# Kernel optimization log

Hardware: AMD Instinct MI355X
Metric: run time of the kernel (lower is better)

The kernel has to match this reference:

```python
import jax, jax.numpy as jnp
import numpy as np
import math

N_GRAPHS = 25
NODES_PER = 2000
N = N_GRAPHS * NODES_PER      # 50000 total nodes
E = 800000                    # total edges
D = 128                       # hidden = out_dim
VOCAB = 30                    # node_len
NLAYERS = 4                   # gcn_num_layers


def setup_inputs() -> dict:
    key = jax.random.key(0)
    ks = jax.random.split(key, 16)
    labels = jax.random.randint(ks[0], (N,), 0, VOCAB)
    src = jax.random.randint(ks[1], (E,), 0, N)
    dst = jax.random.randint(ks[2], (E,), 0, N)
    # true permutations per graph (as the torch code assumes)
    perms = jax.vmap(lambda k: jax.random.permutation(k, NODES_PER))(
        jax.random.split(ks[3], N_GRAPHS))
    s = 0.02
    emb = jax.random.normal(ks[4], (VOCAB, D)) * s
    Ws = jax.random.normal(ks[5], (NLAYERS, D, D)) * s
    bs = jnp.zeros((NLAYERS, D))
    # MLPReadout(D, D) with L=2: D -> D//2 -> D//4 -> D
    w1 = jax.random.normal(ks[6], (D, D // 2)) * s
    b1 = jnp.zeros((D // 2,))
    w2 = jax.random.normal(ks[7], (D // 2, D // 4)) * s
    b2 = jnp.zeros((D // 4,))
    w3 = jax.random.normal(ks[8], (D // 4, D)) * s
    b3 = jnp.zeros((D,))
    return {"labels": labels, "src": src, "dst": dst, "perms": perms,
            "emb": emb, "Ws": Ws, "bs": bs,
            "w1": w1, "b1": b1, "w2": w2, "b2": b2, "w3": w3, "b3": b3}


def _pos_encoding(perms):
    # sinusoidal table [NODES_PER, D]; position starts at 1 per the torch code
    pos = (jnp.arange(NODES_PER, dtype=jnp.float32) + 1.0)[:, None]       # [n,1]
    div = jnp.exp(jnp.arange(0, D, 2, dtype=jnp.float32)
                  * (-math.log(10000.0) / D))                              # [D/2]
    ang = pos * div                                                        # [n,D/2]
    table = jnp.stack([jnp.sin(ang), jnp.cos(ang)], axis=-1).reshape(NODES_PER, D)
    # pes[i][perm_i] = table  (scatter rows per graph)
    pe = jax.vmap(lambda p: jnp.zeros((NODES_PER, D), jnp.float32).at[p].set(table))(perms)
    return pe.reshape(N, D)


def reference(labels, src, dst, perms, emb, Ws, bs, w1, b1, w2, b2, w3, b3):
    h = emb[labels]                                   # embedding lookup [N,D]
    h = h + _pos_encoding(perms)

    ones = jnp.ones((E,), jnp.float32)
    deg_out = jnp.maximum(jax.ops.segment_sum(ones, src, num_segments=N), 1.0)
    deg_in = jnp.maximum(jax.ops.segment_sum(ones, dst, num_segments=N), 1.0)
    isq_src = deg_out ** -0.5                         # DGL GraphConv norm='both'
    isq_dst = deg_in ** -0.5

    for l in range(NLAYERS):
        hn = h * isq_src[:, None]
        m = jax.ops.segment_sum(hn[src], dst, num_segments=N)  # gather-scatter
        m = m * isq_dst[:, None]
        out = jax.nn.relu(m @ Ws[l] + bs[l])
        h = out + h                                   # residual (all dims equal)

    # MLPReadout: D -> D//2 -> D//4 -> D
    x = jax.nn.relu(h @ w1 + b1)
    x = jax.nn.relu(x @ w2 + b2)
    return x @ w3 + b3                                # [N, D]
```

## Files before the change

kernel.cpp:

```cpp
#include <hip/hip_runtime.h>

#define N_NODES 50000
#define N_EDGES 800000
#define D 128
#define NLAYERS 4
#define NODES_PER 2000
#define CAP 64

typedef __attribute__((ext_vector_type(8))) short bf16x8;
typedef __attribute__((ext_vector_type(4))) float f32x4;

__device__ inline unsigned rne16(float f) {
    unsigned u = __float_as_uint(f);
    return (u + 0x7fffu + ((u >> 16) & 1u)) >> 16;
}
__device__ inline unsigned pack_bf2(float a, float b) {
    return rne16(a) | (rne16(b) << 16);
}
__device__ inline float4 bf4_to_f4(uint2 v) {
    float4 r;
    r.x = __uint_as_float(v.x << 16);
    r.y = __uint_as_float(v.x & 0xffff0000u);
    r.z = __uint_as_float(v.y << 16);
    r.w = __uint_as_float(v.y & 0xffff0000u);
    return r;
}

__global__ void build_kernel(const int* __restrict__ src, const int* __restrict__ dst,
                             int* __restrict__ cursor, int* __restrict__ cnt_out_rep,
                             unsigned short* __restrict__ bucket) {
    int e = blockIdx.x * 256 + threadIdx.x;
    if (e < N_EDGES) {
        int s = src[e], d = dst[e];
        atomicAdd(&cnt_out_rep[(blockIdx.x & 3) * N_NODES + s], 1);
        int pos = atomicAdd(&cursor[d], 1);
        if (pos < CAP) bucket[d * CAP + pos] = (unsigned short)s;
    }
}

__global__ void finalize_kernel(const int* __restrict__ cursor,
                                const int* __restrict__ cnt_out_rep,
                                float* __restrict__ isq_src, float* __restrict__ isq_dst) {
    int i = blockIdx.x * 256 + threadIdx.x;
    if (i < N_NODES) {
        int co = cnt_out_rep[i] + cnt_out_rep[N_NODES + i] +
                 cnt_out_rep[2 * N_NODES + i] + cnt_out_rep[3 * N_NODES + i];
        isq_src[i] = rsqrtf((float)max(co, 1));
        isq_dst[i] = rsqrtf((float)max(cursor[i], 1));
    }
}

__global__ void transpose_w_kernel(const float* __restrict__ Ws,
                                   unsigned short* __restrict__ Wt) {
    int l = blockIdx.x;
    const float* W = Ws + (size_t)l * D * D;
    unsigned short* T = Wt + (size_t)l * D * D;
    for (int i = threadIdx.x; i < D * D; i += 256) {
        int k = i >> 7, n = i & 127;
        T[n * D + k] = (unsigned short)rne16(W[i]);
    }
}

__global__ void init_h_kernel(const int* __restrict__ labels, const int* __restrict__ perms,
                              const float* __restrict__ emb, const float* __restrict__ isq_src,
                              float* __restrict__ h, unsigned short* __restrict__ hs16) {
    int b = blockIdx.x;
    int g = b / NODES_PER;
    int i = b - g * NODES_PER;
    int node = g * NODES_PER + perms[b];
    int d = threadIdx.x;
    int k = d >> 1;
    float ang = (float)(i + 1) * expf((float)(2 * k) * (-9.210340371976184f / 128.0f));
    float pe = (d & 1) ? cosf(ang) : sinf(ang);
    float v = emb[labels[node] * D + d] + pe;
    h[node * D + d] = v;
    hs16[node * D + d] = (unsigned short)rne16(v * isq_src[node]);
}

__global__ __launch_bounds__(256) void aggregate_kernel(const unsigned short* __restrict__ hs16,
        const int* __restrict__ cursor, const unsigned short* __restrict__ bucket,
        const float* __restrict__ isq_dst, unsigned short* __restrict__ m16) {
    int node = blockIdx.x * 4 + (threadIdx.x >> 6);
    int lane = threadIdx.x & 63;
    int q = lane >> 4;
    int col = lane & 15;
    int deg = min(cursor[node], CAP);
    int start = node * CAP;
    int end = start + deg;
    const unsigned short* hb = hs16 + col * 8;
    float a[8] = {0.f, 0.f, 0.f, 0.f, 0.f, 0.f, 0.f, 0.f};

    int e = start;
    for (; e + 8 <= end; e += 8) {
        int s0 = bucket[e + q];
        int s1 = bucket[e + 4 + q];
        uint4 v0 = *(const uint4*)&hb[s0 * D];
        uint4 v1 = *(const uint4*)&hb[s1 * D];
        float4 f0 = bf4_to_f4(make_uint2(v0.x, v0.y));
        float4 f1 = bf4_to_f4(make_uint2(v0.z, v0.w));
        float4 f2 = bf4_to_f4(make_uint2(v1.x, v1.y));
        float4 f3 = bf4_to_f4(make_uint2(v1.z, v1.w));
        a[0] += f0.x; a[1] += f0.y; a[2] += f0.z; a[3] += f0.w;
        a[4] += f1.x; a[5] += f1.y; a[6] += f1.z; a[7] += f1.w;
        a[0] += f2.x; a[1] += f2.y; a[2] += f2.z; a[3] += f2.w;
        a[4] += f3.x; a[5] += f3.y; a[6] += f3.z; a[7] += f3.w;
    }
    if (e + 4 <= end) {
        int s0 = bucket[e + q];
        uint4 v0 = *(const uint4*)&hb[s0 * D];
        float4 f0 = bf4_to_f4(make_uint2(v0.x, v0.y));
        float4 f1 = bf4_to_f4(make_uint2(v0.z, v0.w));
        a[0] += f0.x; a[1] += f0.y; a[2] += f0.z; a[3] += f0.w;
        a[4] += f1.x; a[5] += f1.y; a[6] += f1.z; a[7] += f1.w;
        e += 4;
    }
    int r = end - e;
    if (q < r) {
        int s0 = bucket[e + q];
        uint4 v0 = *(const uint4*)&hb[s0 * D];
        float4 f0 = bf4_to_f4(make_uint2(v0.x, v0.y));
        float4 f1 = bf4_to_f4(make_uint2(v0.z, v0.w));
        a[0] += f0.x; a[1] += f0.y; a[2] += f0.z; a[3] += f0.w;
        a[4] += f1.x; a[5] += f1.y; a[6] += f1.z; a[7] += f1.w;
    }
#pragma unroll
    for (int i = 0; i < 8; ++i) {
        a[i] += __shfl_xor(a[i], 16, 64);
        a[i] += __shfl_xor(a[i], 32, 64);
    }
    if (q == 0) {
        float wd = isq_dst[node];
        uint4 o;
        o.x = pack_bf2(a[0] * wd, a[1] * wd);
        o.y = pack_bf2(a[2] * wd, a[3] * wd);
        o.z = pack_bf2(a[4] * wd, a[5] * wd);
        o.w = pack_bf2(a[6] * wd, a[7] * wd);
        *(uint4*)&m16[node * D + col * 8] = o;
    }
}

__global__ __launch_bounds__(256) void layer_mfma_kernel(const unsigned short* __restrict__ m16,
        const unsigned short* __restrict__ Wt, const float* __restrict__ bias,
        float* __restrict__ h, unsigned short* __restrict__ hs16,
        const float* __restrict__ isq) {
    int wave = threadIdx.x >> 6;
    int lane = threadIdx.x & 63;
    int rowbase = blockIdx.x * 64 + wave * 16;
    int col16 = lane & 15;
    int kq8 = (lane >> 4) * 8;

    int arow = min(rowbase + col16, N_NODES - 1);
    bf16x8 afrag[4];
#pragma unroll
    for (int kk = 0; kk < 4; ++kk)
        afrag[kk] = *(const bf16x8*)&m16[(size_t)arow * D + kk * 32 + kq8];

    int orow0 = rowbase + (lane >> 4) * 4;

#pragma unroll 2
    for (int nt = 0; nt < 8; ++nt) {
        int ncol = nt * 16 + col16;
        float bv = bias[ncol];
        f32x4 acc = {bv, bv, bv, bv};
#pragma unroll
        for (int kk = 0; kk < 4; ++kk) {
            bf16x8 bfrag = *(const bf16x8*)&Wt[(size_t)ncol * D + kk * 32 + kq8];
            acc = __builtin_amdgcn_mfma_f32_16x16x32_bf16(afrag[kk], bfrag, acc, 0, 0, 0);
        }
#pragma unroll
        for (int r = 0; r < 4; ++r) {
            int row = orow0 + r;
            if (row < N_NODES) {
                size_t idx = (size_t)row * D + ncol;
                float o = fmaxf(acc[r], 0.f) + h[idx];
                h[idx] = o;
                if (isq) hs16[idx] = (unsigned short)rne16(o * isq[row]);
            }
        }
    }
}

__global__ __launch_bounds__(256, 4) void readout_kernel(const float* __restrict__ h,
        const float* __restrict__ w1, const float* __restrict__ b1,
        const float* __restrict__ w2, const float* __restrict__ b2,
        const float* __restrict__ w3, const float* __restrict__ b3,
        float* __restrict__ out) {
    __shared__ float hT[128][68];
    int t = threadIdx.x;
    int rowbase = blockIdx.x * 64;
    int tx = t & 15, ty = t >> 4;
    int r0 = ty * 4;

    for (int i = t; i < 2048; i += 256) {
        int row = i >> 5;
        int kc = i & 31;
        int grow = rowbase + row;
        float4 v = (grow < N_NODES) ? *(const float4*)&h[grow * D + kc * 4]
                                    : make_float4(0.f, 0.f, 0.f, 0.f);
        int cs = row ^ ((kc & 7) << 2);
        hT[kc * 4 + 0][cs] = v.x;
        hT[kc * 4 + 1][cs] = v.y;
        hT[kc * 4 + 2][cs] = v.z;
        hT[kc * 4 + 3][cs] = v.w;
    }
    __syncthreads();

    float a1[4][4];
    {
        int c1 = tx * 4;
        float4 bv = *(const float4*)&b1[c1];
#pragma unroll
        for (int i = 0; i < 4; ++i) {
            a1[i][0] = bv.x; a1[i][1] = bv.y; a1[i][2] = bv.z; a1[i][3] = bv.w;
        }
#pragma unroll 2
        for (int k = 0; k < 128; ++k) {
            int s4 = ((k >> 2) & 7) << 2;
            float4 ma = *(const float4*)&hT[k][r0 ^ s4];
            float4 wv = *(const float4*)&w1[k * 64 + c1];
            float mv[4] = {ma.x, ma.y, ma.z, ma.w};
#pragma unroll
            for (int i = 0; i < 4; ++i) {
                a1[i][0] += mv[i] * wv.x;
                a1[i][1] += mv[i] * wv.y;
                a1[i][2] += mv[i] * wv.z;
                a1[i][3] += mv[i] * wv.w;
            }
        }
    }
    __syncthreads();
    {
        int c1 = tx * 4;
#pragma unroll
        for (int j = 0; j < 4; ++j) {
            int c = c1 + j;
            int cs = r0 ^ (((c >> 2) & 7) << 2);
            *(float4*)&hT[c][cs] = make_float4(fmaxf(a1[0][j], 0.f), fmaxf(a1[1][j], 0.f),
                                               fmaxf(a1[2][j], 0.f), fmaxf(a1[3][j], 0.f));
        }
    }
    __syncthreads();

    {
        int c2 = tx * 2;
        float a2[4][2];
        float2 bv = *(const float2*)&b2[c2];
#pragma unroll
        for (int i = 0; i < 4; ++i) { a2[i][0] = bv.x; a2[i][1] = bv.y; }
#pragma unroll 2
        for (int k = 0; k < 64; ++k) {
            int s4 = ((k >> 2) & 7) << 2;
            float4 ma = *(const float4*)&hT[k][r0 ^ s4];
            float2 wv = *(const float2*)&w2[k * 32 + c2];
            float mv[4] = {ma.x, ma.y, ma.z, ma.w};
#pragma unroll
            for (int i = 0; i < 4; ++i) {
                a2[i][0] += mv[i] * wv.x;
                a2[i][1] += mv[i] * wv.y;
            }
        }
#pragma unroll
        for (int j = 0; j < 2; ++j) {
            int c = c2 + j;
            int cs = r0 ^ (((c >> 2) & 7) << 2);
            *(float4*)&hT[64 + c][cs] = make_float4(fmaxf(a2[0][j], 0.f), fmaxf(a2[1][j], 0.f),
                                                    fmaxf(a2[2][j], 0.f), fmaxf(a2[3][j], 0.f));
        }
    }
    __syncthreads();

    {
        int c0 = tx * 8;
        float acc[4][8];
        float4 bv0 = *(const float4*)&b3[c0];
        float4 bv1 = *(const float4*)&b3[c0 + 4];
#pragma unroll
        for (int i = 0; i < 4; ++i) {
            acc[i][0] = bv0.x; acc[i][1] = bv0.y; acc[i][2] = bv0.z; acc[i][3] = bv0.w;
            acc[i][4] = bv1.x; acc[i][5] = bv1.y; acc[i][6] = bv1.z; acc[i][7] = bv1.w;
        }
#pragma unroll 4
        for (int k = 0; k < 32; ++k) {
            int s4 = ((k >> 2) & 7) << 2;
            float4 ma = *(const float4*)&hT[64 + k][r0 ^ s4];
            float4 wa = *(const float4*)&w3[k * D + c0];
            float4 wb = *(const float4*)&w3[k * D + c0 + 4];
            float mv[4] = {ma.x, ma.y, ma.z, ma.w};
            float wv[8] = {wa.x, wa.y, wa.z, wa.w, wb.x, wb.y, wb.z, wb.w};
#pragma unroll
            for (int i = 0; i < 4; ++i)
#pragma unroll
                for (int j = 0; j < 8; ++j)
                    acc[i][j] += mv[i] * wv[j];
        }
#pragma unroll
        for (int i = 0; i < 4; ++i) {
            int row = rowbase + r0 + i;
            if (row < N_NODES) {
                *(float4*)&out[row * D + c0] =
                    make_float4(acc[i][0], acc[i][1], acc[i][2], acc[i][3]);
                *(float4*)&out[row * D + c0 + 4] =
                    make_float4(acc[i][4], acc[i][5], acc[i][6], acc[i][7]);
            }
        }
    }
}

extern "C" void kernel_launch(void* const* d_in, const int* in_sizes, int n_in,
                              void* d_out, int out_size, void* d_ws, size_t ws_size,
                              hipStream_t stream) {
    const int*   labels = (const int*)d_in[0];
    const int*   src    = (const int*)d_in[1];
    const int*   dst    = (const int*)d_in[2];
    const int*   perms  = (const int*)d_in[3];
    const float* emb    = (const float*)d_in[4];
    const float* Ws     = (const float*)d_in[5];
    const float* bs     = (const float*)d_in[6];
    const float* w1     = (const float*)d_in[7];
    const float* b1     = (const float*)d_in[8];
    const float* w2     = (const float*)d_in[9];
    const float* b2     = (const float*)d_in[10];
    const float* w3     = (const float*)d_in[11];
    const float* b3     = (const float*)d_in[12];
    float* out = (float*)d_out;

    char* p = (char*)d_ws;
    auto alloc = [&](size_t bytes) -> char* {
        char* r = p;
        p += (bytes + 255) & ~size_t(255);
        return r;
    };
    float*          h       = (float*)alloc((size_t)N_NODES * D * 4);
    unsigned short* hs16    = (unsigned short*)alloc((size_t)N_NODES * D * 2);
    unsigned short* m16     = (unsigned short*)alloc((size_t)N_NODES * D * 2);
    unsigned short* Wt      = (unsigned short*)alloc((size_t)NLAYERS * D * D * 2);
    float*          isq_src = (float*)alloc((size_t)N_NODES * 4);
    float*          isq_dst = (float*)alloc((size_t)N_NODES * 4);
    int*            cursor  = (int*)alloc((size_t)5 * N_NODES * 4);
    int*            cnt_rep = cursor + N_NODES;
    unsigned short* bucket  = (unsigned short*)alloc((size_t)N_NODES * CAP * 2);

    hipMemsetAsync(cursor, 0, (size_t)5 * N_NODES * 4, stream);
    transpose_w_kernel<<<NLAYERS, 256, 0, stream>>>(Ws, Wt);
    build_kernel<<<(N_EDGES + 255) / 256, 256, 0, stream>>>(src, dst, cursor, cnt_rep, bucket);
    finalize_kernel<<<(N_NODES + 255) / 256, 256, 0, stream>>>(cursor, cnt_rep,
                                                               isq_src, isq_dst);
    init_h_kernel<<<N_NODES, 128, 0, stream>>>(labels, perms, emb, isq_src, h, hs16);

    for (int l = 0; l < NLAYERS; ++l) {
        aggregate_kernel<<<N_NODES / 4, 256, 0, stream>>>(hs16, cursor, bucket, isq_dst, m16);
        layer_mfma_kernel<<<(N_NODES + 63) / 64, 256, 0, stream>>>(
            m16, Wt + (size_t)l * D * D, bs + (size_t)l * D, h, hs16,
            (l < NLAYERS - 1) ? isq_src : (const float*)nullptr);
    }
    readout_kernel<<<(N_NODES + 63) / 64, 256, 0, stream>>>(h, w1, b1, w2, b2, w3, b3, out);
}
```

Before: 481.6 us.

## Fuse setup kernels and move readout MLP to bf16 MFMA

After: 455.3 us. -5.5%, faster.

```diff
diff --git a/kernel.cpp b/kernel.cpp
--- a/kernel.cpp
+++ b/kernel.cpp
@@ -6,6 +6,8 @@
 #define NLAYERS 4
 #define NODES_PER 2000
 #define CAP 64
+#define NB_BUILD 3125
+#define NB_INIT 25000
 
 typedef __attribute__((ext_vector_type(8))) short bf16x8;
 typedef __attribute__((ext_vector_type(4))) float f32x4;
@@ -26,15 +28,59 @@
     return r;
 }
 
-__global__ void build_kernel(const int* __restrict__ src, const int* __restrict__ dst,
-                             int* __restrict__ cursor, int* __restrict__ cnt_out_rep,
-                             unsigned short* __restrict__ bucket) {
-    int e = blockIdx.x * 256 + threadIdx.x;
-    if (e < N_EDGES) {
-        int s = src[e], d = dst[e];
-        atomicAdd(&cnt_out_rep[(blockIdx.x & 3) * N_NODES + s], 1);
-        int pos = atomicAdd(&cursor[d], 1);
-        if (pos < CAP) bucket[d * CAP + pos] = (unsigned short)s;
+__global__ void build_init_kernel(const int* __restrict__ src, const int* __restrict__ dst,
+                                  int* __restrict__ cursor, int* __restrict__ cnt_out_rep,
+                                  unsigned short* __restrict__ bucket,
+                                  const int* __restrict__ labels, const int* __restrict__ perms,
+                                  const float* __restrict__ emb, float* __restrict__ h,
+                                  const float* __restrict__ Ws, unsigned short* __restrict__ Wt,
+                                  const float* __restrict__ w1, unsigned short* __restrict__ w1t,
+                                  const float* __restrict__ w2, unsigned short* __restrict__ w2t,
+                                  const float* __restrict__ w3, unsigned short* __restrict__ w3t) {
+    int b = blockIdx.x;
+    if (b < NB_BUILD) {
+        int e = b * 256 + threadIdx.x;
+        if (e < N_EDGES) {
+            int s = src[e], d = dst[e];
+            atomicAdd(&cnt_out_rep[(b & 3) * N_NODES + s], 1);
+            int pos = atomicAdd(&cursor[d], 1);
+            if (pos < CAP) bucket[d * CAP + pos] = (unsigned short)s;
+        }
+    } else if (b < NB_BUILD + NB_INIT) {
+        int j = (b - NB_BUILD) * 2 + (threadIdx.x >> 7);
+        int d = threadIdx.x & 127;
+        int g = j / NODES_PER;
+        int i = j - g * NODES_PER;
+        int node = g * NODES_PER + perms[j];
+        int k = d >> 1;
+        float ang = (float)(i + 1) * expf((float)(2 * k) * (-9.210340371976184f / 128.0f));
+        float pe = (d & 1) ? cosf(ang) : sinf(ang);
+        h[node * D + d] = emb[labels[node] * D + d] + pe;
+    } else {
+        int tb = b - NB_BUILD - NB_INIT;
+        if (tb < NLAYERS) {
+            const float* W = Ws + (size_t)tb * D * D;
+            unsigned short* T = Wt + (size_t)tb * D * D;
+            for (int i = threadIdx.x; i < D * D; i += 256) {
+                int k = i >> 7, n = i & 127;
+                T[n * D + k] = (unsigned short)rne16(W[i]);
+            }
+        } else if (tb == NLAYERS) {
+            for (int i = threadIdx.x; i < 128 * 64; i += 256) {
+                int k = i >> 6, n = i & 63;
+                w1t[n * 128 + k] = (unsigned short)rne16(w1[i]);
+            }
+        } else if (tb == NLAYERS + 1) {
+            for (int i = threadIdx.x; i < 64 * 32; i += 256) {
+                int k = i >> 5, n = i & 31;
+                w2t[n * 64 + k] = (unsigned short)rne16(w2[i]);
+            }
+        } else {
+            for (int i = threadIdx.x; i < 32 * 128; i += 256) {
+                int k = i >> 7, n = i & 127;
+                w3t[n * 32 + k] = (unsigned short)rne16(w3[i]);
+            }
+        }
     }
 }
 
@@ -50,31 +96,21 @@
     }
 }
 
-__global__ void transpose_w_kernel(const float* __restrict__ Ws,
-                                   unsigned short* __restrict__ Wt) {
-    int l = blockIdx.x;
-    const float* W = Ws + (size_t)l * D * D;
-    unsigned short* T = Wt + (size_t)l * D * D;
-    for (int i = threadIdx.x; i < D * D; i += 256) {
-        int k = i >> 7, n = i & 127;
-        T[n * D + k] = (unsigned short)rne16(W[i]);
-    }
-}
-
-__global__ void init_h_kernel(const int* __restrict__ labels, const int* __restrict__ perms,
-                              const float* __restrict__ emb, const float* __restrict__ isq_src,
-                              float* __restrict__ h, unsigned short* __restrict__ hs16) {
-    int b = blockIdx.x;
-    int g = b / NODES_PER;
-    int i = b - g * NODES_PER;
-    int node = g * NODES_PER + perms[b];
-    int d = threadIdx.x;
-    int k = d >> 1;
-    float ang = (float)(i + 1) * expf((float)(2 * k) * (-9.210340371976184f / 128.0f));
-    float pe = (d & 1) ? cosf(ang) : sinf(ang);
-    float v = emb[labels[node] * D + d] + pe;
-    h[node * D + d] = v;
-    hs16[node * D + d] = (unsigned short)rne16(v * isq_src[node]);
+__global__ void hs16_kernel(const float* __restrict__ h, const float* __restrict__ isq_src,
+                            unsigned short* __restrict__ hs16) {
+    int gid = blockIdx.x * 256 + threadIdx.x;
+    int row = gid >> 4;
+    int c8 = (gid & 15) * 8;
+    float s = isq_src[row];
+    size_t idx = (size_t)row * D + c8;
+    float4 v0 = *(const float4*)&h[idx];
+    float4 v1 = *(const float4*)&h[idx + 4];
+    uint4 o;
+    o.x = pack_bf2(v0.x * s, v0.y * s);
+    o.y = pack_bf2(v0.z * s, v0.w * s);
+    o.z = pack_bf2(v1.x * s, v1.y * s);
+    o.w = pack_bf2(v1.z * s, v1.w * s);
+    *(uint4*)&hs16[idx] = o;
 }
 
 __global__ __launch_bounds__(256) void aggregate_kernel(const unsigned short* __restrict__ hs16,
@@ -174,134 +210,79 @@
                 size_t idx = (size_t)row * D + ncol;
                 float o = fmaxf(acc[r], 0.f) + h[idx];
                 h[idx] = o;
-                if (isq) hs16[idx] = (unsigned short)rne16(o * isq[row]);
-            }
-        }
-    }
-}
-
-__global__ __launch_bounds__(256, 4) void readout_kernel(const float* __restrict__ h,
-        const float* __restrict__ w1, const float* __restrict__ b1,
-        const float* __restrict__ w2, const float* __restrict__ b2,
-        const float* __restrict__ w3, const float* __restrict__ b3,
+                float s = isq ? isq[row] : 1.0f;
+                hs16[idx] = (unsigned short)rne16(o * s);
+            }
+        }
+    }
+}
+
+__global__ __launch_bounds__(256) void readout_mfma_kernel(const unsigned short* __restrict__ h16,
+        const unsigned short* __restrict__ w1t, const float* __restrict__ b1,
+        const unsigned short* __restrict__ w2t, const float* __restrict__ b2,
+        const unsigned short* __restrict__ w3t, const float* __restrict__ b3,
         float* __restrict__ out) {
-    __shared__ float hT[128][68];
-    int t = threadIdx.x;
-    int rowbase = blockIdx.x * 64;
-    int tx = t & 15, ty = t >> 4;
-    int r0 = ty * 4;
-
-    for (int i = t; i < 2048; i += 256) {
-        int row = i >> 5;
-        int kc = i & 31;
-        int grow = rowbase + row;
-        float4 v = (grow < N_NODES) ? *(const float4*)&h[grow * D + kc * 4]
-                                    : make_float4(0.f, 0.f, 0.f, 0.f);
-        int cs = row ^ ((kc & 7) << 2);
-        hT[kc * 4 + 0][cs] = v.x;
-        hT[kc * 4 + 1][cs] = v.y;
-        hT[kc * 4 + 2][cs] = v.z;
-        hT[kc * 4 + 3][cs] = v.w;
-    }
-    __syncthreads();
-
-    float a1[4][4];
-    {
-        int c1 = tx * 4;
-        float4 bv = *(const float4*)&b1[c1];
-#pragma unroll
-        for (int i = 0; i < 4; ++i) {
-            a1[i][0] = bv.x; a1[i][1] = bv.y; a1[i][2] = bv.z; a1[i][3] = bv.w;
-        }
+    __shared__ __align__(16) unsigned short y1s[4][16][72];
+    __shared__ __align__(16) unsigned short y2s[4][16][40];
+    int wave = threadIdx.x >> 6;
+    int lane = threadIdx.x & 63;
+    int rowbase = blockIdx.x * 64 + wave * 16;
+    int c16 = lane & 15;
+    int kq8 = (lane >> 4) * 8;
+    int rt0 = (lane >> 4) * 4;
+
+    int arow = min(rowbase + c16, N_NODES - 1);
+    bf16x8 af[4];
+#pragma unroll
+    for (int kk = 0; kk < 4; ++kk)
+        af[kk] = *(const bf16x8*)&h16[(size_t)arow * D + kk * 32 + kq8];
+
+#pragma unroll
+    for (int nt = 0; nt < 4; ++nt) {
+        int ncol = nt * 16 + c16;
+        float bv = b1[ncol];
+        f32x4 acc = {bv, bv, bv, bv};
+#pragma unroll
+        for (int kk = 0; kk < 4; ++kk) {
+            bf16x8 bfrag = *(const bf16x8*)&w1t[(size_t)ncol * 128 + kk * 32 + kq8];
+            acc = __builtin_amdgcn_mfma_f32_16x16x32_bf16(af[kk], bfrag, acc, 0, 0, 0);
+        }
+#pragma unroll
+        for (int r = 0; r < 4; ++r)
+            y1s[wave][rt0 + r][ncol] = (unsigned short)rne16(fmaxf(acc[r], 0.f));
+    }
+
+    bf16x8 a2[2];
+#pragma unroll
+    for (int kk = 0; kk < 2; ++kk)
+        a2[kk] = *(const bf16x8*)&y1s[wave][c16][kk * 32 + kq8];
+#pragma unroll
+    for (int nt = 0; nt < 2; ++nt) {
+        int ncol = nt * 16 + c16;
+        float bv = b2[ncol];
+        f32x4 acc = {bv, bv, bv, bv};
+#pragma unroll
+        for (int kk = 0; kk < 2; ++kk) {
+            bf16x8 bfrag = *(const bf16x8*)&w2t[(size_t)ncol * 64 + kk * 32 + kq8];
+            acc = __builtin_amdgcn_mfma_f32_16x16x32_bf16(a2[kk], bfrag, acc, 0, 0, 0);
+        }
+#pragma unroll
+        for (int r = 0; r < 4; ++r)
+            y2s[wave][rt0 + r][ncol] = (unsigned short)rne16(fmaxf(acc[r], 0.f));
+    }
+
+    bf16x8 a3 = *(const bf16x8*)&y2s[wave][c16][kq8];
 #pragma unroll 2
-        for (int k = 0; k < 128; ++k) {
-            int s4 = ((k >> 2) & 7) << 2;
-            float4 ma = *(const float4*)&hT[k][r0 ^ s4];
-            float4 wv = *(const float4*)&w1[k * 64 + c1];
-            float mv[4] = {ma.x, ma.y, ma.z, ma.w};
-#pragma unroll
-            for (int i = 0; i < 4; ++i) {
-                a1[i][0] += mv[i] * wv.x;
-                a1[i][1] += mv[i] * wv.y;
-                a1[i][2] += mv[i] * wv.z;
-                a1[i][3] += mv[i] * wv.w;
-            }
-        }
-    }
-    __syncthreads();
-    {
-        int c1 = tx * 4;
-#pragma unroll
-        for (int j = 0; j < 4; ++j) {
-            int c = c1 + j;
-            int cs = r0 ^ (((c >> 2) & 7) << 2);
-            *(float4*)&hT[c][cs] = make_float4(fmaxf(a1[0][j], 0.f), fmaxf(a1[1][j], 0.f),
-                                               fmaxf(a1[2][j], 0.f), fmaxf(a1[3][j], 0.f));
-        }
-    }
-    __syncthreads();
-
-    {
-        int c2 = tx * 2;
-        float a2[4][2];
-        float2 bv = *(const float2*)&b2[c2];
-#pragma unroll
-        for (int i = 0; i < 4; ++i) { a2[i][0] = bv.x; a2[i][1] = bv.y; }
-#pragma unroll 2
-        for (int k = 0; k < 64; ++k) {
-            int s4 = ((k >> 2) & 7) << 2;
-            float4 ma = *(const float4*)&hT[k][r0 ^ s4];
-            float2 wv = *(const float2*)&w2[k * 32 + c2];
-            float mv[4] = {ma.x, ma.y, ma.z, ma.w};
-#pragma unroll
-            for (int i = 0; i < 4; ++i) {
-                a2[i][0] += mv[i] * wv.x;
-                a2[i][1] += mv[i] * wv.y;
-            }
-        }
-#pragma unroll
-        for (int j = 0; j < 2; ++j) {
-            int c = c2 + j;
-            int cs = r0 ^ (((c >> 2) & 7) << 2);
-            *(float4*)&hT[64 + c][cs] = make_float4(fmaxf(a2[0][j], 0.f), fmaxf(a2[1][j], 0.f),
-                                                    fmaxf(a2[2][j], 0.f), fmaxf(a2[3][j], 0.f));
-        }
-    }
-    __syncthreads();
-
-    {
-        int c0 = tx * 8;
-        float acc[4][8];
-        float4 bv0 = *(const float4*)&b3[c0];
-        float4 bv1 = *(const float4*)&b3[c0 + 4];
-#pragma unroll
-        for (int i = 0; i < 4; ++i) {
-            acc[i][0] = bv0.x; acc[i][1] = bv0.y; acc[i][2] = bv0.z; acc[i][3] = bv0.w;
-            acc[i][4] = bv1.x; acc[i][5] = bv1.y; acc[i][6] = bv1.z; acc[i][7] = bv1.w;
-        }
-#pragma unroll 4
-        for (int k = 0; k < 32; ++k) {
-            int s4 = ((k >> 2) & 7) << 2;
-            float4 ma = *(const float4*)&hT[64 + k][r0 ^ s4];
-            float4 wa = *(const float4*)&w3[k * D + c0];
-            float4 wb = *(const float4*)&w3[k * D + c0 + 4];
-            float mv[4] = {ma.x, ma.y, ma.z, ma.w};
-            float wv[8] = {wa.x, wa.y, wa.z, wa.w, wb.x, wb.y, wb.z, wb.w};
-#pragma unroll
-            for (int i = 0; i < 4; ++i)
-#pragma unroll
-                for (int j = 0; j < 8; ++j)
-                    acc[i][j] += mv[i] * wv[j];
-        }
-#pragma unroll
-        for (int i = 0; i < 4; ++i) {
-            int row = rowbase + r0 + i;
-            if (row < N_NODES) {
-                *(float4*)&out[row * D + c0] =
-                    make_float4(acc[i][0], acc[i][1], acc[i][2], acc[i][3]);
-                *(float4*)&out[row * D + c0 + 4] =
-                    make_float4(acc[i][4], acc[i][5], acc[i][6], acc[i][7]);
-            }
+    for (int nt = 0; nt < 8; ++nt) {
+        int ncol = nt * 16 + c16;
+        float bv = b3[ncol];
+        f32x4 acc = {bv, bv, bv, bv};
+        bf16x8 bfrag = *(const bf16x8*)&w3t[(size_t)ncol * 32 + kq8];
+        acc = __builtin_amdgcn_mfma_f32_16x16x32_bf16(a3, bfrag, acc, 0, 0, 0);
+#pragma unroll
+        for (int r = 0; r < 4; ++r) {
+            int row = rowbase + rt0 + r;
+            if (row < N_NODES) out[(size_t)row * D + ncol] = acc[r];
         }
     }
 }
@@ -334,6 +315,9 @@
     unsigned short* hs16    = (unsigned short*)alloc((size_t)N_NODES * D * 2);
     unsigned short* m16     = (unsigned short*)alloc((size_t)N_NODES * D * 2);
     unsigned short* Wt      = (unsigned short*)alloc((size_t)NLAYERS * D * D * 2);
+    unsigned short* w1t     = (unsigned short*)alloc((size_t)64 * 128 * 2);
+    unsigned short* w2t     = (unsigned short*)alloc((size_t)32 * 64 * 2);
+    unsigned short* w3t     = (unsigned short*)alloc((size_t)128 * 32 * 2);
     float*          isq_src = (float*)alloc((size_t)N_NODES * 4);
     float*          isq_dst = (float*)alloc((size_t)N_NODES * 4);
     int*            cursor  = (int*)alloc((size_t)5 * N_NODES * 4);
@@ -341,11 +325,13 @@
     unsigned short* bucket  = (unsigned short*)alloc((size_t)N_NODES * CAP * 2);
 
     hipMemsetAsync(cursor, 0, (size_t)5 * N_NODES * 4, stream);
-    transpose_w_kernel<<<NLAYERS, 256, 0, stream>>>(Ws, Wt);
-    build_kernel<<<(N_EDGES + 255) / 256, 256, 0, stream>>>(src, dst, cursor, cnt_rep, bucket);
+    build_init_kernel<<<NB_BUILD + NB_INIT + NLAYERS + 3, 256, 0, stream>>>(
+        src, dst, cursor, cnt_rep, bucket,
+        labels, perms, emb, h,
+        Ws, Wt, w1, w1t, w2, w2t, w3, w3t);
     finalize_kernel<<<(N_NODES + 255) / 256, 256, 0, stream>>>(cursor, cnt_rep,
                                                                isq_src, isq_dst);
-    init_h_kernel<<<N_NODES, 128, 0, stream>>>(labels, perms, emb, isq_src, h, hs16);
+    hs16_kernel<<<3125, 256, 0, stream>>>(h, isq_src, hs16);
 
     for (int l = 0; l < NLAYERS; ++l) {
         aggregate_kernel<<<N_NODES / 4, 256, 0, stream>>>(hs16, cursor, bucket, isq_dst, m16);
@@ -353,5 +339,6 @@
             m16, Wt + (size_t)l * D * D, bs + (size_t)l * D, h, hs16,
             (l < NLAYERS - 1) ? isq_src : (const float*)nullptr);
     }
-    readout_kernel<<<(N_NODES + 63) / 64, 256, 0, stream>>>(h, w1, b1, w2, b2, w3, b3, out);
-}
+    readout_mfma_kernel<<<(N_NODES + 63) / 64, 256, 0, stream>>>(
+        hs16, w1t, b1, w2t, b2, w3t, b3, out);
+}
```
